# Kernel tuning notes

Measured on AMD Instinct MI355X. Metric: run time of the kernel, lower is better.

The kernel has to match this reference:

```python
import jax, jax.numpy as jnp
import numpy as np

NUM_EMBEDDINGS = 1024
EMBEDDING_SIZE = 256
COMMITMENT_COST = 0.25


def setup_inputs() -> dict:
    key = jax.random.key(0)
    kx, kw = jax.random.split(key)
    x = jax.random.normal(kx, (16, EMBEDDING_SIZE, 64, 64), dtype=jnp.float32)
    # nn.Embedding init: uniform(-1/K, 1/K)
    w = jax.random.uniform(kw, (NUM_EMBEDDINGS, EMBEDDING_SIZE), dtype=jnp.float32,
                           minval=-1.0 / NUM_EMBEDDINGS, maxval=1.0 / NUM_EMBEDDINGS)
    return {"x": x, "w": w}


def reference(x, w):
    # x: [B, C, H, W] -> NHWC
    xh = jnp.transpose(x, (0, 2, 3, 1))  # [B, H, W, D]
    B, H, W, D = xh.shape
    x_flat = xh.reshape(-1, D)  # [N, D]
    distances = (jnp.sum(x_flat * x_flat, axis=1, keepdims=True)
                 + jnp.sum(w * w, axis=1)
                 - 2.0 * (x_flat @ w.T))  # [N, K]
    indices_flat = jnp.argmin(distances, axis=1)  # [N]
    quantized = w[indices_flat].reshape(B, H, W, D)
    indices = indices_flat.reshape(B, H, W)[:, None, :, :]  # [B,1,H,W]
    # training-mode losses
    e_latent_loss = jnp.mean((jax.lax.stop_gradient(quantized) - xh) ** 2)
    q_latent_loss = jnp.mean((quantized - jax.lax.stop_gradient(xh)) ** 2)
    loss = q_latent_loss + COMMITMENT_COST * e_latent_loss
    # straight-through estimator
    quantized = xh + jax.lax.stop_gradient(quantized - xh)
    quantized = jnp.transpose(quantized, (0, 3, 1, 2))  # back to NCHW
    return quantized, indices, loss
```

## Files before the change

kernel.cpp:

```cpp
#include <hip/hip_runtime.h>
#include <math.h>

#define NUM_K 1024
#define DIM 256
#define HW 4096
#define NPIX 65536
#define QELEMS 16777216
#define MAX_FLAGS 16384

typedef short bf16x8 __attribute__((ext_vector_type(8)));
typedef float f32x4 __attribute__((ext_vector_type(4)));

__device__ __forceinline__ unsigned short f32_to_bf16_rne(float f) {
    unsigned int u = __float_as_uint(f);
    unsigned int r = u + 0x7FFFu + ((u >> 16) & 1u);
    return (unsigned short)(r >> 16);
}
__device__ __forceinline__ float bf16_to_f32(unsigned short h) {
    return __uint_as_float(((unsigned int)h) << 16);
}

__device__ __forceinline__ void merge3(float& a1d, int& a1i, float& a2d, int& a2i, float& a3d,
                                       float b1d, int b1i, float b2d, int b2i, float b3d) {
    bool bf = (b1d < a1d) || (b1d == a1d && b1i < a1i);
    float r1d = bf ? b1d : a1d; int r1i = bf ? b1i : a1i;
    float n2d = bf ? b2d : a2d; int n2i = bf ? b2i : a2i;
    float o1d = bf ? a1d : b1d; int o1i = bf ? a1i : b1i;
    bool k2 = (n2d < o1d) || (n2d == o1d && n2i < o1i);
    float r2d = k2 ? n2d : o1d; int r2i = k2 ? n2i : o1i;
    float sm3 = bf ? b3d : a3d;
    float o2d = bf ? a2d : b2d;
    float r3d = k2 ? fminf(sm3, o1d) : fminf(n2d, o2d);
    a1d = r1d; a1i = r1i; a2d = r2d; a2i = r2i; a3d = r3d;
}

__device__ __forceinline__ float np_sumsq_256(const float* __restrict__ p, long stride) {
    float blk0 = 0.f, blk1 = 0.f;
#pragma unroll
    for (int h = 0; h < 2; ++h) {
        const float* base = p + (long)h * 128 * stride;
        float s[16];
#pragma unroll
        for (int L = 0; L < 16; ++L) {
            float a0 = base[(long)(L)       * stride]; a0 = __fmul_rn(a0, a0);
            float a1 = base[(long)(16 + L)  * stride]; a1 = __fmul_rn(a1, a1);
            float a2 = base[(long)(32 + L)  * stride]; a2 = __fmul_rn(a2, a2);
            float a3 = base[(long)(48 + L)  * stride]; a3 = __fmul_rn(a3, a3);
            float a4 = base[(long)(64 + L)  * stride]; a4 = __fmul_rn(a4, a4);
            float a5 = base[(long)(80 + L)  * stride]; a5 = __fmul_rn(a5, a5);
            float a6 = base[(long)(96 + L)  * stride]; a6 = __fmul_rn(a6, a6);
            float a7 = base[(long)(112 + L) * stride]; a7 = __fmul_rn(a7, a7);
            float t1 = __fadd_rn(a0, a1);
            float t2 = __fadd_rn(a2, a3);
            float t3 = __fadd_rn(a4, a5);
            float t4 = __fadd_rn(a6, a7);
            s[L] = __fadd_rn(__fadd_rn(t1, t2), __fadd_rn(t3, t4));
        }
        float c0 = __fadd_rn(s[0], s[8]);
        float c1 = __fadd_rn(s[1], s[9]);
        float c2 = __fadd_rn(s[2], s[10]);
        float c3 = __fadd_rn(s[3], s[11]);
        float c4 = __fadd_rn(s[4], s[12]);
        float c5 = __fadd_rn(s[5], s[13]);
        float c6 = __fadd_rn(s[6], s[14]);
        float c7 = __fadd_rn(s[7], s[15]);
        float d0 = __fadd_rn(c0, c4);
        float d1 = __fadd_rn(c1, c5);
        float d2 = __fadd_rn(c2, c6);
        float d3 = __fadd_rn(c3, c7);
        float e0 = __fadd_rn(d0, d2);
        float e1 = __fadd_rn(d1, d3);
        float r  = __fadd_rn(e0, e1);
        if (h == 0) blk0 = r; else blk1 = r;
    }
    return __fadd_rn(blk0, blk1);
}

__global__ __launch_bounds__(256) void k_wsq(const float* __restrict__ w, float* __restrict__ wsq) {
    int k = blockIdx.x * 256 + threadIdx.x;
    if (k < NUM_K) wsq[k] = np_sumsq_256(w + (long)k * DIM, 1);
}

__global__ __launch_bounds__(256) void k_xsq(const float* __restrict__ x, float* __restrict__ xsq) {
    int n = blockIdx.x * 256 + threadIdx.x;
    int b = n >> 12, hw = n & 4095;
    xsq[n] = np_sumsq_256(x + (long)b * DIM * HW + hw, HW);
}

__global__ __launch_bounds__(1024)
void k_wtrans(const float* __restrict__ w, float* __restrict__ wtr) {
    int d = blockIdx.x;
    int k = threadIdx.x;
    wtr[(long)d * NUM_K + k] = w[(long)k * DIM + d];
}

__global__ __launch_bounds__(256)
void k_wfrag(const float* __restrict__ w, short* __restrict__ whi) {
    int id = blockIdx.x * 256 + threadIdx.x;
    int code = id >> 5;
    int c = id & 31;
    const float* src = w + (long)code * DIM + c * 8;
    bf16x8 vh;
#pragma unroll
    for (int j = 0; j < 8; ++j) vh[j] = (short)f32_to_bf16_rne(src[j]);
    int fl = ((c & 3) << 4) | (code & 15);
    long addr = ((((long)(code >> 4) * 8 + (c >> 2)) * 64 + fl) * 8);
    *(bf16x8*)(whi + addr) = vh;
}

#define A_SLOT(ks,m,fl) ((((ks)*4+(m))*64+(fl))*8)

__global__ __launch_bounds__(256, 2)
void k_argmin_mfma(const float* __restrict__ x,
                   const short* __restrict__ whi,
                   const float* __restrict__ wsq, const float* __restrict__ xsq,
                   float* __restrict__ pd1, int* __restrict__ pi1,
                   float* __restrict__ pd2, int* __restrict__ pi2,
                   float* __restrict__ pd3) {
    __shared__ short ahi[8 * 4 * 64 * 8];
    __shared__ short alo[8 * 4 * 64 * 8];
    __shared__ float cd1[4][64], cd2[4][64], cd3[4][64];
    __shared__ int   ci1[4][64], ci2[4][64];

    const int t = threadIdx.x;
    const int lane = t & 63;
    const int q = t >> 6;
    const int tile = blockIdx.x >> 1;
    const int slice = blockIdx.x & 1;

    const int b = tile >> 6;
    const int hw0 = (tile & 63) * 64;
    const float* xb = x + (long)b * (DIM * HW) + hw0 + lane;

#pragma unroll
    for (int i = 0; i < 8; ++i) {
        int c = q * 8 + i;
        float v[8];
#pragma unroll
        for (int jj = 0; jj < 8; ++jj) v[jj] = xb[(long)(c * 8 + jj) * HW];
        bf16x8 vh, vl;
#pragma unroll
        for (int jj = 0; jj < 8; ++jj) {
            unsigned short hh = f32_to_bf16_rne(v[jj]);
            float r = __fsub_rn(v[jj], bf16_to_f32(hh));
            vh[jj] = (short)hh;
            vl[jj] = (short)f32_to_bf16_rne(r);
        }
        int slot = A_SLOT(c >> 2, lane >> 4, ((c & 3) << 4) | (lane & 15));
        *(bf16x8*)(ahi + slot) = vh;
        *(bf16x8*)(alo + slot) = vl;
    }
    __syncthreads();

    const int ct0 = slice * 32 + q * 8;
    f32x4 acc[4][8];
#pragma unroll
    for (int m = 0; m < 4; ++m)
#pragma unroll
        for (int n = 0; n < 8; ++n) acc[m][n] = (f32x4){0.f, 0.f, 0.f, 0.f};

#define BADDR(i) ((((long)(ct0 + ((i) & 7)) * 8 + ((i) >> 3)) * 64 + lane) * 8)
    bf16x8 bring[4];
#pragma unroll
    for (int i = 0; i < 4; ++i) bring[i] = *(const bf16x8*)(whi + BADDR(i));

    bf16x8 ah[4], al[4];
#pragma unroll
    for (int i = 0; i < 64; ++i) {
        const int ks = i >> 3;
        const int n = i & 7;
        if (n == 0) {
#pragma unroll
            for (int m = 0; m < 4; ++m) {
                ah[m] = *(const bf16x8*)(ahi + A_SLOT(ks, m, lane));
                al[m] = *(const bf16x8*)(alo + A_SLOT(ks, m, lane));
            }
        }
        bf16x8 bcur = bring[i & 3];
        if (i + 4 < 64) bring[i & 3] = *(const bf16x8*)(whi + BADDR(i + 4));
#pragma unroll
        for (int m = 0; m < 4; ++m) {
            acc[m][n] = __builtin_amdgcn_mfma_f32_16x16x32_bf16(ah[m], bcur, acc[m][n], 0, 0, 0);
            acc[m][n] = __builtin_amdgcn_mfma_f32_16x16x32_bf16(al[m], bcur, acc[m][n], 0, 0, 0);
        }
    }
#undef BADDR

    const long px0 = (long)tile * 64;
    const int rbase = (lane >> 4) * 4;
    float s1v[4][4];
#pragma unroll
    for (int m = 0; m < 4; ++m)
#pragma unroll
        for (int r = 0; r < 4; ++r) s1v[m][r] = xsq[px0 + 16 * m + rbase + r];

    float e1d[4][4], e2d[4][4], e3d[4][4];
    int   e1i[4][4], e2i[4][4];
#pragma unroll
    for (int m = 0; m < 4; ++m)
#pragma unroll
        for (int r = 0; r < 4; ++r) {
            e1d[m][r] = INFINITY; e2d[m][r] = INFINITY; e3d[m][r] = INFINITY;
            e1i[m][r] = 0; e2i[m][r] = 0;
        }

#pragma unroll
    for (int n = 0; n < 8; ++n) {
        int code = (ct0 + n) * 16 + (lane & 15);
        float wq = wsq[code];
#pragma unroll
        for (int m = 0; m < 4; ++m) {
#pragma unroll
            for (int r = 0; r < 4; ++r) {
                float tt = __fadd_rn(s1v[m][r], wq);
                float dist = __fmaf_rn(-2.0f, acc[m][n][r], tt);
                bool c1 = dist < e1d[m][r];
                bool c2 = dist < e2d[m][r];
                bool c3 = dist < e3d[m][r];
                float n3 = c2 ? e2d[m][r] : (c3 ? dist : e3d[m][r]);
                float n2 = c1 ? e1d[m][r] : (c2 ? dist : e2d[m][r]);
                int   j2 = c1 ? e1i[m][r] : (c2 ? code : e2i[m][r]);
                float n1 = c1 ? dist : e1d[m][r];
                int   j1 = c1 ? code : e1i[m][r];
                e3d[m][r] = n3; e2d[m][r] = n2; e2i[m][r] = j2;
                e1d[m][r] = n1; e1i[m][r] = j1;
            }
        }
    }

#pragma unroll
    for (int step = 1; step < 16; step <<= 1) {
#pragma unroll
        for (int m = 0; m < 4; ++m) {
#pragma unroll
            for (int r = 0; r < 4; ++r) {
                float o1 = __shfl_xor(e1d[m][r], step);
                int   p1 = __shfl_xor(e1i[m][r], step);
                float o2 = __shfl_xor(e2d[m][r], step);
                int   p2 = __shfl_xor(e2i[m][r], step);
                float o3 = __shfl_xor(e3d[m][r], step);
                merge3(e1d[m][r], e1i[m][r], e2d[m][r], e2i[m][r], e3d[m][r],
                       o1, p1, o2, p2, o3);
            }
        }
    }

    if ((lane & 15) == 0) {
#pragma unroll
        for (int m = 0; m < 4; ++m) {
#pragma unroll
            for (int r = 0; r < 4; ++r) {
                int px = 16 * m + rbase + r;
                cd1[q][px] = e1d[m][r]; ci1[q][px] = e1i[m][r];
                cd2[q][px] = e2d[m][r]; ci2[q][px] = e2i[m][r];
                cd3[q][px] = e3d[m][r];
            }
        }
    }
    __syncthreads();

    if (t < 64) {
        float d1 = cd1[0][t], d2 = cd2[0][t], d3 = cd3[0][t];
        int   i1 = ci1[0][t], i2 = ci2[0][t];
#pragma unroll
        for (int s = 1; s < 4; ++s) {
            merge3(d1, i1, d2, i2, d3, cd1[s][t], ci1[s][t], cd2[s][t], ci2[s][t], cd3[s][t]);
        }
        long n = (long)slice * NPIX + px0 + t;
        pd1[n] = d1; pi1[n] = i1; pd2[n] = d2; pi2[n] = i2; pd3[n] = d3;
    }
}

__global__ __launch_bounds__(256)
void k_combine(const float* __restrict__ pd1, const int* __restrict__ pi1,
               const float* __restrict__ pd2, const int* __restrict__ pi2,
               const float* __restrict__ pd3, int* __restrict__ idx,
               int4* __restrict__ pairf, int* __restrict__ paircnt,
               int* __restrict__ fullf, int* __restrict__ fullcnt) {
    int n = blockIdx.x * 256 + threadIdx.x;
    float d1 = pd1[n], d2 = pd2[n], d3 = pd3[n];
    int   i1 = pi1[n], i2 = pi2[n];
    long n1 = (long)NPIX + n;
    merge3(d1, i1, d2, i2, d3, pd1[n1], pi1[n1], pd2[n1], pi2[n1], pd3[n1]);
    idx[n] = i1;
    float m = d1 * 1.0e-6f;
    if (__fsub_rn(d3, d1) <= m) {
        int pos = atomicAdd(fullcnt, 1);
        if (pos < MAX_FLAGS) fullf[pos] = n;
    } else if (__fsub_rn(d2, d1) <= m) {
        int pos = atomicAdd(paircnt, 1);
        if (pos < MAX_FLAGS) pairf[pos] = (int4){n, i1, i2, 0};
    }
}

__global__ __launch_bounds__(256, 2)
void k_argmin_valu(const float* __restrict__ x, const float* __restrict__ w,
                   const float* __restrict__ wsq, const float* __restrict__ xsq,
                   int* __restrict__ idx, int* __restrict__ fullf, int* __restrict__ fullcnt) {
    __shared__ float xs[64 * 257];
    __shared__ float sd1[4][64];
    __shared__ float sd2[4][64];
    __shared__ int   si1[4][64];

    const int t = threadIdx.x;
    const int p = t & 63;
    const int q = t >> 6;
    const long n0 = (long)blockIdx.x * 64;
    const int b = (int)(n0 >> 12);
    const int hw0 = (int)(n0 & 4095);
    const float* xb = x + (long)b * DIM * HW + hw0;

    for (int i = 0; i < 64; ++i) {
        int c = q * 64 + i;
        xs[p * 257 + c] = xb[(long)c * HW + p];
    }
    __syncthreads();

    const float* xrow = xs + p * 257;
    const float s1 = xsq[n0 + p];
    float d1 = INFINITY, d2 = INFINITY;
    int i1 = 0;
    const int kbase = q * 256;
    const float* wq = w + (long)kbase * DIM;
    const float* wsq_q = wsq + kbase;

    for (int kc = 0; kc < 256; kc += 8) {
        float acc[8] = {0.f, 0.f, 0.f, 0.f, 0.f, 0.f, 0.f, 0.f};
        const float* w0 = wq + (long)kc * DIM;
#pragma unroll 2
        for (int d = 0; d < DIM; d += 4) {
            float x0 = xrow[d + 0];
            float x1 = xrow[d + 1];
            float x2 = xrow[d + 2];
            float x3 = xrow[d + 3];
#pragma unroll
            for (int j = 0; j < 8; ++j) {
                const float4 wv = *reinterpret_cast<const float4*>(w0 + j * DIM + d);
                acc[j] = __fmaf_rn(x0, wv.x, acc[j]);
                acc[j] = __fmaf_rn(x1, wv.y, acc[j]);
                acc[j] = __fmaf_rn(x2, wv.z, acc[j]);
                acc[j] = __fmaf_rn(x3, wv.w, acc[j]);
            }
        }
#pragma unroll
        for (int j = 0; j < 8; ++j) {
            float tk = __fadd_rn(s1, wsq_q[kc + j]);
            float dist = __fsub_rn(tk, __fmul_rn(2.0f, acc[j]));
            if (dist < d1) { d2 = d1; d1 = dist; i1 = kbase + kc + j; }
            else if (dist < d2) { d2 = dist; }
        }
    }

    sd1[q][p] = d1; sd2[q][p] = d2; si1[q][p] = i1;
    __syncthreads();
    if (q == 0) {
        float bd1 = sd1[0][p], bd2 = sd2[0][p];
        int bi = si1[0][p];
#pragma unroll
        for (int j = 1; j < 4; ++j) {
            float a1 = sd1[j][p], a2 = sd2[j][p];
            int ai = si1[j][p];
            if (a1 < bd1) { bd2 = fminf(bd1, a2); bd1 = a1; bi = ai; }
            else { bd2 = fminf(bd2, fminf(a1, a2)); }
        }
        const long n = n0 + p;
        idx[n] = bi;
        if (__fsub_rn(bd2, bd1) <= bd1 * 6.0e-7f) {
            int pos = atomicAdd(fullcnt, 1);
            if (pos < MAX_FLAGS) fullf[pos] = (int)n;
        }
    }
}

__global__ __launch_bounds__(256)
void k_refine_pair(const float* __restrict__ x, const float* __restrict__ w,
                   const float* __restrict__ wsq, const float* __restrict__ xsq,
                   const int4* __restrict__ pairf, const int* __restrict__ paircnt,
                   int* __restrict__ idx) {
    int np = *paircnt;
    if (np > MAX_FLAGS) np = MAX_FLAGS;
    const int lane = threadIdx.x & 63;
    const int wv = threadIdx.x >> 6;
    for (int fi = blockIdx.x * 4 + wv; fi < np; fi += gridDim.x * 4) {
        int4 f = pairf[fi];
        int n = f.x, c1 = f.y, c2 = f.z;
        int b = n >> 12, hw = n & 4095;
        const float* xp = x + (long)b * (DIM * HW) + hw;
        double xd0 = (double)xp[(long)(lane * 4 + 0) * HW];
        double xd1 = (double)xp[(long)(lane * 4 + 1) * HW];
        double xd2 = (double)xp[(long)(lane * 4 + 2) * HW];
        double xd3 = (double)xp[(long)(lane * 4 + 3) * HW];
        const float4 w1 = *reinterpret_cast<const float4*>(w + (long)c1 * DIM + lane * 4);
        const float4 w2 = *reinterpret_cast<const float4*>(w + (long)c2 * DIM + lane * 4);
        double s1 = fma((double)w1.x, xd0, fma((double)w1.y, xd1,
                    fma((double)w1.z, xd2, (double)w1.w * xd3)));
        double s2 = fma((double)w2.x, xd0, fma((double)w2.y, xd1,
                    fma((double)w2.z, xd2, (double)w2.w * xd3)));
#pragma unroll
        for (int st = 1; st < 64; st <<= 1) {
            s1 += __shfl_xor(s1, st);
            s2 += __shfl_xor(s2, st);
        }
        if (lane == 0) {
            float xq = xsq[n];
            float dk1 = __fsub_rn(__fadd_rn(xq, wsq[c1]), __fmul_rn(2.0f, (float)s1));
            float dk2 = __fsub_rn(__fadd_rn(xq, wsq[c2]), __fmul_rn(2.0f, (float)s2));
            bool take2 = (dk2 < dk1) || (dk2 == dk1 && c2 < c1);
            idx[n] = take2 ? c2 : c1;
        }
    }
}

__global__ __launch_bounds__(1024)
void k_refine_full(const float* __restrict__ x, const float* __restrict__ wtr,
                   const float* __restrict__ wsq, const float* __restrict__ xsq,
                   const int* __restrict__ fullf, const int* __restrict__ fullcnt,
                   int* __restrict__ idx) {
    __shared__ float xsf[DIM][4];
    __shared__ int   np_s[4];
    __shared__ float s1_s[4];
    __shared__ float wd[16][4];
    __shared__ int   wi[16][4];

    int nf = *fullcnt;
    if (nf > MAX_FLAGS) nf = MAX_FLAGS;
    const int t = threadIdx.x;
    const int lane = t & 63;
    const int wid = t >> 6;

    for (int base = blockIdx.x * 4; base < nf; base += gridDim.x * 4) {
        __syncthreads();
        if (t < 4) {
            int fi = base + t;
            int n = fullf[fi < nf ? fi : (nf - 1)];
            np_s[t] = n;
            s1_s[t] = xsq[n];
        }
        __syncthreads();
        {
            int p = t & 3, d = t >> 2;
            int n = np_s[p];
            xsf[d][p] = x[(long)(n >> 12) * (DIM * HW) + (long)d * HW + (n & 4095)];
        }
        __syncthreads();

        const float wq = wsq[t];
        double a0 = 0.0, a1 = 0.0, a2 = 0.0, a3 = 0.0;
#pragma unroll 4
        for (int d = 0; d < DIM; ++d) {
            double wk = (double)wtr[(long)d * NUM_K + t];
            float4 xv = *reinterpret_cast<const float4*>(&xsf[d][0]);
            a0 = fma(wk, (double)xv.x, a0);
            a1 = fma(wk, (double)xv.y, a1);
            a2 = fma(wk, (double)xv.z, a2);
            a3 = fma(wk, (double)xv.w, a3);
        }
        float dkv[4];
        int   kiv[4];
        dkv[0] = __fsub_rn(__fadd_rn(s1_s[0], wq), __fmul_rn(2.0f, (float)a0));
        dkv[1] = __fsub_rn(__fadd_rn(s1_s[1], wq), __fmul_rn(2.0f, (float)a1));
        dkv[2] = __fsub_rn(__fadd_rn(s1_s[2], wq), __fmul_rn(2.0f, (float)a2));
        dkv[3] = __fsub_rn(__fadd_rn(s1_s[3], wq), __fmul_rn(2.0f, (float)a3));
#pragma unroll
        for (int p = 0; p < 4; ++p) kiv[p] = t;

#pragma unroll
        for (int step = 1; step < 64; step <<= 1) {
#pragma unroll
            for (int p = 0; p < 4; ++p) {
                float od = __shfl_xor(dkv[p], step);
                int   oi = __shfl_xor(kiv[p], step);
                if (od < dkv[p] || (od == dkv[p] && oi < kiv[p])) { dkv[p] = od; kiv[p] = oi; }
            }
        }
        if (lane == 0) {
#pragma unroll
            for (int p = 0; p < 4; ++p) { wd[wid][p] = dkv[p]; wi[wid][p] = kiv[p]; }
        }
        __syncthreads();
        if (t < 4) {
            float bd = wd[0][t];
            int   bi = wi[0][t];
#pragma unroll
            for (int s = 1; s < 16; ++s) {
                float ad = wd[s][t];
                int   ai = wi[s][t];
                if (ad < bd || (ad == bd && ai < bi)) { bd = ad; bi = ai; }
            }
            if (base + t < nf) idx[np_s[t]] = bi;
        }
    }
}

__global__ __launch_bounds__(256, 2)
void k_quant(const float* __restrict__ x, const float* __restrict__ w,
             const int* __restrict__ idx, float* __restrict__ qout,
             float* __restrict__ iout, float* __restrict__ loss) {
    __shared__ float wrow[64 * 257];
    __shared__ int lidx[64];
    __shared__ float part[4];
    const int t = threadIdx.x;
    const long n0 = (long)blockIdx.x * 64;
    const int b = (int)(n0 >> 12), hw0 = (int)(n0 & 4095);

    if (t < 64) lidx[t] = idx[n0 + t];
    __syncthreads();
    for (int i = 0; i < 64; ++i) {
        wrow[i * 257 + t] = w[(long)lidx[i] * DIM + t];
    }
    if (t < 64) iout[n0 + t] = (float)lidx[t];
    __syncthreads();

    const int p = t & 63, cg = t >> 6;
    const float* xb = x + (long)b * DIM * HW + hw0;
    float* qb = qout + (long)b * DIM * HW + hw0;
    float lsum = 0.f;
    for (int i = 0; i < 64; ++i) {
        int c = cg * 64 + i;
        float qv = wrow[p * 257 + c];
        long off = (long)c * HW + p;
        float xv = xb[off];
        float diff = __fsub_rn(qv, xv);
        qb[off] = __fadd_rn(xv, diff);
        lsum = __fmaf_rn(diff, diff, lsum);
    }
#pragma unroll
    for (int off = 32; off; off >>= 1) lsum += __shfl_down(lsum, off);
    if ((t & 63) == 0) part[t >> 6] = lsum;
    __syncthreads();
    if (t == 0) {
        float tot = (part[0] + part[1]) + (part[2] + part[3]);
        atomicAdd(loss, tot * (1.25f / 16777216.f));
    }
}

extern "C" void kernel_launch(void* const* d_in, const int* in_sizes, int n_in,
                              void* d_out, int out_size, void* d_ws, size_t ws_size,
                              hipStream_t stream) {
    const float* x = (const float*)d_in[0];
    const float* w = (const float*)d_in[1];

    float* qout = (float*)d_out;
    float* iout = qout + QELEMS;
    float* loss = iout + NPIX;

    char* wp = (char*)d_ws;
    int*   idx     = (int*)wp;      wp += (size_t)NPIX * 4;
    float* wsq     = (float*)wp;    wp += (size_t)NUM_K * 4;
    float* xsq     = (float*)wp;    wp += (size_t)NPIX * 4;
    int4*  pairf   = (int4*)wp;     wp += (size_t)MAX_FLAGS * 16;
    int*   paircnt = (int*)wp;      wp += 256;
    int*   fullf   = (int*)wp;      wp += (size_t)MAX_FLAGS * 4;
    int*   fullcnt = (int*)wp;      wp += 256;
    float* wtr     = (float*)wp;    wp += (size_t)NUM_K * DIM * 4;
    short* whi     = (short*)wp;    wp += (size_t)NUM_K * DIM * 2;
    float* pd1     = (float*)wp;    wp += (size_t)2 * NPIX * 4;
    int*   pi1     = (int*)wp;      wp += (size_t)2 * NPIX * 4;
    float* pd2     = (float*)wp;    wp += (size_t)2 * NPIX * 4;
    int*   pi2     = (int*)wp;      wp += (size_t)2 * NPIX * 4;
    float* pd3     = (float*)wp;    wp += (size_t)2 * NPIX * 4;
    size_t need = (size_t)(wp - (char*)d_ws);

    hipMemsetAsync(loss, 0, sizeof(float), stream);
    hipMemsetAsync(paircnt, 0, sizeof(int), stream);
    hipMemsetAsync(fullcnt, 0, sizeof(int), stream);

    k_wsq<<<4, 256, 0, stream>>>(w, wsq);
    k_xsq<<<NPIX / 256, 256, 0, stream>>>(x, xsq);
    k_wtrans<<<DIM, 1024, 0, stream>>>(w, wtr);

    if (ws_size >= need) {
        k_wfrag<<<128, 256, 0, stream>>>(w, whi);
        k_argmin_mfma<<<2048, 256, 0, stream>>>(x, whi, wsq, xsq, pd1, pi1, pd2, pi2, pd3);
        k_combine<<<NPIX / 256, 256, 0, stream>>>(pd1, pi1, pd2, pi2, pd3, idx,
                                                  pairf, paircnt, fullf, fullcnt);
        k_refine_pair<<<2048, 256, 0, stream>>>(x, w, wsq, xsq, pairf, paircnt, idx);
    } else {
        k_argmin_valu<<<NPIX / 64, 256, 0, stream>>>(x, w, wsq, xsq, idx, fullf, fullcnt);
    }
    k_refine_full<<<1024, 1024, 0, stream>>>(x, wtr, wsq, xsq, fullf, fullcnt, idx);
    k_quant<<<NPIX / 64, 256, 0, stream>>>(x, w, idx, qout, iout, loss);
}
```

Before: 237.0 us.

## Drop split-bf16 low part in MFMA argmin, widen refine margin and batching

The MFMA distance pass now uses a single bf16 rounding of x instead of a hi+lo split. This halves the MFMA count and the shared-memory A staging, and the occupancy hint is raised to 4 blocks. To make up for the lower precision, the near-tie flag margin grows from 1e-6 to 2.5e-6 relative, so more pixels go to the exact refine passes. The full refine kernel now handles 8 pixels per block instead of 4 on a half-size grid. Risk: more flagged pixels may overflow MAX_FLAGS, or true winners may be missed if the bf16 error exceeds the margin.

Result: slower. 808.4 us (+241.1%).

```diff
diff --git a/kernel.cpp b/kernel.cpp
--- a/kernel.cpp
+++ b/kernel.cpp
@@ -110,7 +110,7 @@
 
 #define A_SLOT(ks,m,fl) ((((ks)*4+(m))*64+(fl))*8)
 
-__global__ __launch_bounds__(256, 2)
+__global__ __launch_bounds__(256, 4)
 void k_argmin_mfma(const float* __restrict__ x,
                    const short* __restrict__ whi,
                    const float* __restrict__ wsq, const float* __restrict__ xsq,
@@ -118,7 +118,6 @@
                    float* __restrict__ pd2, int* __restrict__ pi2,
                    float* __restrict__ pd3) {
     __shared__ short ahi[8 * 4 * 64 * 8];
-    __shared__ short alo[8 * 4 * 64 * 8];
     __shared__ float cd1[4][64], cd2[4][64], cd3[4][64];
     __shared__ int   ci1[4][64], ci2[4][64];
 
@@ -138,17 +137,11 @@
         float v[8];
 #pragma unroll
         for (int jj = 0; jj < 8; ++jj) v[jj] = xb[(long)(c * 8 + jj) * HW];
-        bf16x8 vh, vl;
-#pragma unroll
-        for (int jj = 0; jj < 8; ++jj) {
-            unsigned short hh = f32_to_bf16_rne(v[jj]);
-            float r = __fsub_rn(v[jj], bf16_to_f32(hh));
-            vh[jj] = (short)hh;
-            vl[jj] = (short)f32_to_bf16_rne(r);
-        }
+        bf16x8 vh;
+#pragma unroll
+        for (int jj = 0; jj < 8; ++jj) vh[jj] = (short)f32_to_bf16_rne(v[jj]);
         int slot = A_SLOT(c >> 2, lane >> 4, ((c & 3) << 4) | (lane & 15));
         *(bf16x8*)(ahi + slot) = vh;
-        *(bf16x8*)(alo + slot) = vl;
     }
     __syncthreads();
 
@@ -164,25 +157,21 @@
 #pragma unroll
     for (int i = 0; i < 4; ++i) bring[i] = *(const bf16x8*)(whi + BADDR(i));
 
-    bf16x8 ah[4], al[4];
+    bf16x8 ah[4];
 #pragma unroll
     for (int i = 0; i < 64; ++i) {
         const int ks = i >> 3;
         const int n = i & 7;
         if (n == 0) {
 #pragma unroll
-            for (int m = 0; m < 4; ++m) {
+            for (int m = 0; m < 4; ++m)
                 ah[m] = *(const bf16x8*)(ahi + A_SLOT(ks, m, lane));
-                al[m] = *(const bf16x8*)(alo + A_SLOT(ks, m, lane));
-            }
         }
         bf16x8 bcur = bring[i & 3];
         if (i + 4 < 64) bring[i & 3] = *(const bf16x8*)(whi + BADDR(i + 4));
 #pragma unroll
-        for (int m = 0; m < 4; ++m) {
+        for (int m = 0; m < 4; ++m)
             acc[m][n] = __builtin_amdgcn_mfma_f32_16x16x32_bf16(ah[m], bcur, acc[m][n], 0, 0, 0);
-            acc[m][n] = __builtin_amdgcn_mfma_f32_16x16x32_bf16(al[m], bcur, acc[m][n], 0, 0, 0);
-        }
     }
 #undef BADDR
 
@@ -283,7 +272,7 @@
     long n1 = (long)NPIX + n;
     merge3(d1, i1, d2, i2, d3, pd1[n1], pi1[n1], pd2[n1], pi2[n1], pd3[n1]);
     idx[n] = i1;
-    float m = d1 * 1.0e-6f;
+    float m = d1 * 2.5e-6f;
     if (__fsub_rn(d3, d1) <= m) {
         int pos = atomicAdd(fullcnt, 1);
         if (pos < MAX_FLAGS) fullf[pos] = n;
@@ -416,11 +405,11 @@
                    const float* __restrict__ wsq, const float* __restrict__ xsq,
                    const int* __restrict__ fullf, const int* __restrict__ fullcnt,
                    int* __restrict__ idx) {
-    __shared__ float xsf[DIM][4];
-    __shared__ int   np_s[4];
-    __shared__ float s1_s[4];
-    __shared__ float wd[16][4];
-    __shared__ int   wi[16][4];
+    __shared__ float xsf[DIM][8];
+    __shared__ int   np_s[8];
+    __shared__ float s1_s[8];
+    __shared__ float wd[16][8];
+    __shared__ int   wi[16][8];
 
     int nf = *fullcnt;
     if (nf > MAX_FLAGS) nf = MAX_FLAGS;
@@ -428,46 +417,43 @@
     const int lane = t & 63;
     const int wid = t >> 6;
 
-    for (int base = blockIdx.x * 4; base < nf; base += gridDim.x * 4) {
+    for (int base = blockIdx.x * 8; base < nf; base += gridDim.x * 8) {
         __syncthreads();
-        if (t < 4) {
+        if (t < 8) {
             int fi = base + t;
             int n = fullf[fi < nf ? fi : (nf - 1)];
             np_s[t] = n;
             s1_s[t] = xsq[n];
         }
         __syncthreads();
-        {
-            int p = t & 3, d = t >> 2;
+#pragma unroll
+        for (int e = t; e < 2048; e += 1024) {
+            int p = e & 7, d = e >> 3;
             int n = np_s[p];
             xsf[d][p] = x[(long)(n >> 12) * (DIM * HW) + (long)d * HW + (n & 4095)];
         }
         __syncthreads();
 
         const float wq = wsq[t];
-        double a0 = 0.0, a1 = 0.0, a2 = 0.0, a3 = 0.0;
+        double acc[8] = {0.0, 0.0, 0.0, 0.0, 0.0, 0.0, 0.0, 0.0};
 #pragma unroll 4
         for (int d = 0; d < DIM; ++d) {
             double wk = (double)wtr[(long)d * NUM_K + t];
-            float4 xv = *reinterpret_cast<const float4*>(&xsf[d][0]);
-            a0 = fma(wk, (double)xv.x, a0);
-            a1 = fma(wk, (double)xv.y, a1);
-            a2 = fma(wk, (double)xv.z, a2);
-            a3 = fma(wk, (double)xv.w, a3);
-        }
-        float dkv[4];
-        int   kiv[4];
-        dkv[0] = __fsub_rn(__fadd_rn(s1_s[0], wq), __fmul_rn(2.0f, (float)a0));
-        dkv[1] = __fsub_rn(__fadd_rn(s1_s[1], wq), __fmul_rn(2.0f, (float)a1));
-        dkv[2] = __fsub_rn(__fadd_rn(s1_s[2], wq), __fmul_rn(2.0f, (float)a2));
-        dkv[3] = __fsub_rn(__fadd_rn(s1_s[3], wq), __fmul_rn(2.0f, (float)a3));
-#pragma unroll
-        for (int p = 0; p < 4; ++p) kiv[p] = t;
-
+#pragma unroll
+            for (int p = 0; p < 8; ++p) acc[p] = fma(wk, (double)xsf[d][p], acc[p]);
+        }
+
+        float dkv[8];
+        int   kiv[8];
+#pragma unroll
+        for (int p = 0; p < 8; ++p) {
+            dkv[p] = __fsub_rn(__fadd_rn(s1_s[p], wq), __fmul_rn(2.0f, (float)acc[p]));
+            kiv[p] = t;
+        }
 #pragma unroll
         for (int step = 1; step < 64; step <<= 1) {
 #pragma unroll
-            for (int p = 0; p < 4; ++p) {
+            for (int p = 0; p < 8; ++p) {
                 float od = __shfl_xor(dkv[p], step);
                 int   oi = __shfl_xor(kiv[p], step);
                 if (od < dkv[p] || (od == dkv[p] && oi < kiv[p])) { dkv[p] = od; kiv[p] = oi; }
@@ -475,10 +461,10 @@
         }
         if (lane == 0) {
 #pragma unroll
-            for (int p = 0; p < 4; ++p) { wd[wid][p] = dkv[p]; wi[wid][p] = kiv[p]; }
+            for (int p = 0; p < 8; ++p) { wd[wid][p] = dkv[p]; wi[wid][p] = kiv[p]; }
         }
         __syncthreads();
-        if (t < 4) {
+        if (t < 8) {
             float bd = wd[0][t];
             int   bi = wi[0][t];
 #pragma unroll
@@ -578,6 +564,6 @@
     } else {
         k_argmin_valu<<<NPIX / 64, 256, 0, stream>>>(x, w, wsq, xsq, idx, fullf, fullcnt);
     }
-    k_refine_full<<<1024, 1024, 0, stream>>>(x, wtr, wsq, xsq, fullf, fullcnt, idx);
+    k_refine_full<<<512, 1024, 0, stream>>>(x, wtr, wsq, xsq, fullf, fullcnt, idx);
     k_quant<<<NPIX / 64, 256, 0, stream>>>(x, w, idx, qout, iout, loss);
 }
```
